# Optimization experiments

Hardware: AMD Instinct MI355X
Metric: run time of the kernel (lower is better)

The kernel has to match this reference:

```python
import jax, jax.numpy as jnp
import numpy as np

N_HEADS = 16
ROPE_BASE = 10000.0


def _apply_rope(t, cos, sin):
    # t: (B, H, S, D); cos/sin: (S, D/2). Rotate-half convention.
    d2 = t.shape[-1] // 2
    t1, t2 = t[..., :d2], t[..., d2:]
    return jnp.concatenate([t1 * cos - t2 * sin, t2 * cos + t1 * sin], axis=-1)


def setup_inputs() -> dict:
    key = jax.random.key(0)
    k0, k1, k2, k3, k4 = jax.random.split(key, 5)
    B, S, E = 4, 2048, 1024
    scale = 0.02
    x = jax.random.normal(k0, (B, S, E), dtype=jnp.float32)
    w_qkv = jax.random.normal(k1, (E, 3 * E), dtype=jnp.float32) * scale
    b_qkv = jnp.zeros((3 * E,), dtype=jnp.float32)
    w_proj = jax.random.normal(k2, (E, E), dtype=jnp.float32) * scale
    b_proj = jnp.zeros((E,), dtype=jnp.float32)
    return {"x": x, "w_qkv": w_qkv, "b_qkv": b_qkv, "w_proj": w_proj, "b_proj": b_proj}


def reference(x, w_qkv, b_qkv, w_proj, b_proj):
    B, S, E = x.shape
    H = N_HEADS
    D = E // H
    # fused QKV projection
    qkv = x @ w_qkv + b_qkv                      # (B, S, 3E)
    q, k, v = jnp.split(qkv, 3, axis=-1)
    def to_heads(t):
        return t.reshape(B, S, H, D).transpose(0, 2, 1, 3)  # (B, H, S, D)
    q, k, v = to_heads(q), to_heads(k), to_heads(v)
    # RoPE (rotate-half)
    inv_freq = ROPE_BASE ** (-jnp.arange(0, D, 2, dtype=jnp.float32) / D)  # (D/2,)
    pos = jnp.arange(S, dtype=jnp.float32)
    freqs = pos[:, None] * inv_freq[None, :]     # (S, D/2)
    cos, sin = jnp.cos(freqs), jnp.sin(freqs)
    q = _apply_rope(q, cos, sin)
    k = _apply_rope(k, cos, sin)
    # causal SDPA
    scores = jnp.einsum('bhqd,bhkd->bhqk', q, k) / jnp.sqrt(jnp.float32(D))
    causal = jnp.tril(jnp.ones((S, S), dtype=bool))
    scores = jnp.where(causal, scores, jnp.float32(-1e30))
    probs = jax.nn.softmax(scores, axis=-1)
    out = jnp.einsum('bhqk,bhkd->bhqd', probs, v)  # (B, H, S, D)
    out = out.transpose(0, 2, 1, 3).reshape(B, S, E)
    # output projection (dropout is identity at p=0 / eval)
    return out @ w_proj + b_proj
```

## Files before the change

### kernel.cpp

```cpp
#include <hip/hip_runtime.h>

typedef unsigned short u16;
typedef __bf16 bf16x8 __attribute__((ext_vector_type(8)));
typedef float f32x4 __attribute__((ext_vector_type(4)));

__device__ __forceinline__ u16 f2b(float f) {
    unsigned u = __builtin_bit_cast(unsigned, f);
    unsigned r = (u + 0x7fffu + ((u >> 16) & 1u)) >> 16;
    return (u16)r;
}
#if __has_builtin(__builtin_amdgcn_cvt_pk_bf16_f32)
typedef __bf16 bf16x2_t __attribute__((ext_vector_type(2)));
__device__ __forceinline__ unsigned pk2(float a, float b) {
    return __builtin_bit_cast(unsigned, __builtin_amdgcn_cvt_pk_bf16_f32(a, b));
}
#else
__device__ __forceinline__ unsigned pk2(float a, float b) {
    return (unsigned)f2b(a) | ((unsigned)f2b(b) << 16);
}
#endif
#if __has_builtin(__builtin_amdgcn_exp2f)
#define EXP2F(x) __builtin_amdgcn_exp2f(x)
#else
#define EXP2F(x) exp2f(x)
#endif

__device__ __forceinline__ void gl_lds16(const u16* g, u16* l) {
    __builtin_amdgcn_global_load_lds(
        (const __attribute__((address_space(1))) unsigned*)(const void*)g,
        (__attribute__((address_space(3))) unsigned*)(void*)l, 16, 0, 0);
}

__global__ __launch_bounds__(256) void k_rope_table(float2* __restrict__ tab) {
    int i = blockIdx.x * 256 + threadIdx.x;
    int s = i >> 5, d = i & 31;
    const float C0 = 0.4152410118609203f;
    float inv_freq = exp2f(-C0 * (float)d);
    float sn, cs;
    sincosf((float)s * inv_freq, &sn, &cs);
    tab[i] = make_float2(cs, sn);
}

__global__ __launch_bounds__(256) void k_convert(const float* __restrict__ in,
                                                 u16* __restrict__ out, int n8) {
    int i = blockIdx.x * 256 + threadIdx.x;
    if (i >= n8) return;
    const float4* p = (const float4*)(in + (size_t)i * 8);
    float4 a = p[0], b = p[1];
    u16 t[8] = {f2b(a.x), f2b(a.y), f2b(a.z), f2b(a.w),
                f2b(b.x), f2b(b.y), f2b(b.z), f2b(b.w)};
    *(uint4*)(out + (size_t)i * 8) = *(const uint4*)t;
}

__global__ __launch_bounds__(256) void k_transpose_bf16(const float* __restrict__ in,
                                                        u16* __restrict__ out,
                                                        int R, int C) {
    __shared__ u16 tile[64][72];
    int tc = blockIdx.x * 64;
    int tr = blockIdx.y * 64;
    for (int i = threadIdx.x; i < 4096; i += 256) {
        int r = i >> 6, c = i & 63;
        tile[c][r] = f2b(in[(size_t)(tr + r) * C + tc + c]);
    }
    __syncthreads();
    for (int i = threadIdx.x; i < 4096; i += 256) {
        int r = i >> 6, c = i & 63;
        out[(size_t)(tc + r) * R + tr + c] = tile[r][c];
    }
}

__device__ __forceinline__ void gemm_mainloop(const u16* __restrict__ Ab,
                                              const u16* __restrict__ Bb, int K,
                                              u16* As, u16* Bs, int tid,
                                              f32x4 (&acc)[4][4]) {
    const int wave = tid >> 6, lane = tid & 63;
    const int col = lane & 15, quad = lane >> 4;
    const int wm = wave >> 1, wn = wave & 1;
    const int lrow = lane >> 2, lk = (lane & 3) * 8;
    u16* ldsA0 = As + (wave * 16) * 32;
    u16* ldsA1 = As + (64 + wave * 16) * 32;
    u16* ldsB0 = Bs + (wave * 16) * 32;
    u16* ldsB1 = Bs + (64 + wave * 16) * 32;
    const u16* gA0 = Ab + (size_t)(wave * 16 + lrow) * K + lk;
    const u16* gA1 = gA0 + (size_t)64 * K;
    const u16* gB0 = Bb + (size_t)(wave * 16 + lrow) * K + lk;
    const u16* gB1 = gB0 + (size_t)64 * K;
    for (int k0 = 0; k0 < K; k0 += 64) {
        if (k0) __syncthreads();
#pragma unroll
        for (int kh = 0; kh < 2; ++kh) {
            int ko = k0 + kh * 32;
            gl_lds16(gA0 + ko, ldsA0 + kh * 4096);
            gl_lds16(gA1 + ko, ldsA1 + kh * 4096);
            gl_lds16(gB0 + ko, ldsB0 + kh * 4096);
            gl_lds16(gB1 + ko, ldsB1 + kh * 4096);
        }
        __syncthreads();
#pragma unroll
        for (int kh = 0; kh < 2; ++kh) {
            bf16x8 af[4], bfr[4];
#pragma unroll
            for (int mt = 0; mt < 4; ++mt)
                af[mt] = *(const bf16x8*)(As + kh * 4096 +
                                          (wm * 64 + mt * 16 + col) * 32 + quad * 8);
#pragma unroll
            for (int nt = 0; nt < 4; ++nt)
                bfr[nt] = *(const bf16x8*)(Bs + kh * 4096 +
                                           (wn * 64 + nt * 16 + col) * 32 + quad * 8);
#pragma unroll
            for (int mt = 0; mt < 4; ++mt)
#pragma unroll
                for (int nt = 0; nt < 4; ++nt)
                    acc[mt][nt] = __builtin_amdgcn_mfma_f32_16x16x32_bf16(
                        af[mt], bfr[nt], acc[mt][nt], 0, 0, 0);
        }
    }
}

__global__ __launch_bounds__(256) void k_gemm_qkv_rope(
    const u16* __restrict__ A, const u16* __restrict__ Bt,
    const float* __restrict__ bias, const float2* __restrict__ tab,
    u16* __restrict__ Qr, u16* __restrict__ Kr, u16* __restrict__ Vt) {
    __shared__ __align__(16) u16 smem[16384];
    u16* As = smem;
    u16* Bs = smem + 8192;
    const int K = 1024;
    int tid = threadIdx.x;
    int lane = tid & 63, wave = tid >> 6;
    int col = lane & 15, quad = lane >> 4;
    int wm = wave >> 1, wn = wave & 1;
    int mBase = blockIdx.y * 128;
    int nBase = blockIdx.x * 128;
    f32x4 acc[4][4] = {};
    gemm_mainloop(A + (size_t)mBase * K, Bt + (size_t)nBase * K, K, As, Bs, tid, acc);

    int region = nBase >> 10;
    int n64 = nBase + wn * 64;
    int h = (n64 & 1023) >> 6;
    if (region < 2) {
        __syncthreads();
        float qs = (region == 0) ? 0.18033688011112042f : 1.0f;
#pragma unroll
        for (int nt = 0; nt < 2; ++nt) {
            int d1 = nt * 16 + col;
            float b1 = bias[n64 + d1];
            float b2 = bias[n64 + d1 + 32];
            int nl = wn * 64 + nt * 16 + col;
#pragma unroll
            for (int mt = 0; mt < 4; ++mt) {
                int mlb = wm * 64 + mt * 16 + quad * 4;
#pragma unroll
                for (int r = 0; r < 4; ++r) {
                    int mloc = mlb + r;
                    int s = (mBase + mloc) & 2047;
                    float2 t = tab[s * 32 + d1];
                    float t1 = acc[mt][nt][r] + b1;
                    float t2 = acc[mt][nt + 2][r] + b2;
                    int sw = (mloc & 7) << 3;
                    smem[mloc * 128 + (nl ^ sw)] = f2b((t1 * t.x - t2 * t.y) * qs);
                    smem[mloc * 128 + ((nl + 32) ^ sw)] = f2b((t2 * t.x + t1 * t.y) * qs);
                }
            }
        }
        __syncthreads();
        u16* outp = (region == 0) ? Qr : Kr;
#pragma unroll
        for (int p = 0; p < 8; ++p) {
            int lin = p * 256 + tid;
            int mloc = lin >> 4;
            int c8 = (lin & 15) << 3;
            uint4 v = *(const uint4*)(smem + mloc * 128 + (c8 ^ ((mloc & 7) << 3)));
            int m = mBase + mloc;
            int s = m & 2047, b = m >> 11;
            int ng = (nBase & 1023) + c8;
            *(uint4*)(Qr == outp || Kr == outp
                          ? outp + ((size_t)((b * 16 + (ng >> 6)) * 2048 + s)) * 64 +
                                (ng & 63)
                          : outp) = v;
        }
    } else {
        int b = mBase >> 11;
        int sb0 = mBase & 2047;
#pragma unroll
        for (int nt = 0; nt < 4; ++nt) {
            int d = nt * 16 + col;
            float bv = bias[n64 + d];
            u16* vrow = Vt + ((size_t)((b * 16 + h) * 64 + d)) * 2048;
#pragma unroll
            for (int mt = 0; mt < 4; ++mt) {
                int s = sb0 + wm * 64 + mt * 16 + quad * 4;
                uint2 w;
                w.x = pk2(acc[mt][nt][0] + bv, acc[mt][nt][1] + bv);
                w.y = pk2(acc[mt][nt][2] + bv, acc[mt][nt][3] + bv);
                *(uint2*)(vrow + s) = w;
            }
        }
    }
}

__global__ __launch_bounds__(256) void k_attn(const u16* __restrict__ Qr,
                                              const u16* __restrict__ Kr,
                                              const u16* __restrict__ Vt,
                                              u16* __restrict__ O) {
    __shared__ __align__(16) u16 Ks[64 * 72];
    __shared__ __align__(16) u16 Vs[64 * 72];
    int tid = threadIdx.x, wave = tid >> 6, lane = tid & 63;
    int col = lane & 15, quad = lane >> 4;
    int bx = blockIdx.x, bh = blockIdx.y;
    int b = bh >> 4, h = bh & 15;
    size_t headQ = (size_t)bh * 2048 * 64;
    size_t headV = (size_t)bh * 64 * 2048;
    int r0 = tid >> 3, kc = tid & 7;
    int rb72 = ((col >> 2) * 8 + (col & 3)) * 72;

    for (int half = 0; half < 2; ++half) {
        int qb = half ? bx : (15 - bx);
        int t0 = 2 * qb, t1 = t0 + 1;
        int myq0 = qb * 128 + wave * 16 + col;
        int myq1 = myq0 + 64;
        const u16* qp0 = Qr + headQ + (size_t)myq0 * 64;
        const u16* qp1 = Qr + headQ + (size_t)myq1 * 64;
        bf16x8 aq00 = *(const bf16x8*)(qp0 + quad * 8);
        bf16x8 aq01 = *(const bf16x8*)(qp0 + 32 + quad * 8);
        bf16x8 aq10 = *(const bf16x8*)(qp1 + quad * 8);
        bf16x8 aq11 = *(const bf16x8*)(qp1 + 32 + quad * 8);
        f32x4 o0[4] = {}, o1[4] = {};
        float l0 = 0.f, l1 = 0.f;

        for (int j = 0; j <= t1; ++j) {
            bool d0 = (j <= t0);
            __syncthreads();
            {
                const u16* kg = Kr + headQ + (size_t)(j * 64 + r0) * 64 + kc * 8;
                const u16* vg = Vt + headV + (size_t)r0 * 2048 + j * 64 + kc * 8;
                *(uint4*)(Ks + r0 * 72 + kc * 8) = *(const uint4*)kg;
                *(uint4*)(Ks + (r0 + 32) * 72 + kc * 8) = *(const uint4*)(kg + 32 * 64);
                *(uint4*)(Vs + r0 * 72 + kc * 8) = *(const uint4*)vg;
                *(uint4*)(Vs + (r0 + 32) * 72 + kc * 8) = *(const uint4*)(vg + 32 * 2048);
            }
            __syncthreads();
            f32x4 s0[4], s1[4];
#pragma unroll
            for (int nt = 0; nt < 4; ++nt) {
                const u16* kp = Ks + rb72 + ((nt & 1) * 32 + (nt >> 1) * 4) * 72;
                bf16x8 ak0 = *(const bf16x8*)(kp + quad * 8);
                bf16x8 ak1 = *(const bf16x8*)(kp + 32 + quad * 8);
                if (d0) {
                    f32x4 z = {};
                    z = __builtin_amdgcn_mfma_f32_16x16x32_bf16(ak0, aq00, z, 0, 0, 0);
                    s0[nt] = __builtin_amdgcn_mfma_f32_16x16x32_bf16(ak1, aq01, z, 0, 0, 0);
                }
                f32x4 z = {};
                z = __builtin_amdgcn_mfma_f32_16x16x32_bf16(ak0, aq10, z, 0, 0, 0);
                s1[nt] = __builtin_amdgcn_mfma_f32_16x16x32_bf16(ak1, aq11, z, 0, 0, 0);
            }
            if (j == t0) {
#pragma unroll
                for (int nt = 0; nt < 4; ++nt) {
                    int keyb = j * 64 + (nt & 1) * 32 + quad * 8 + (nt >> 1) * 4;
#pragma unroll
                    for (int r = 0; r < 4; ++r)
                        if (keyb + r > myq0) s0[nt][r] = -3.0e38f;
                }
            }
            if (j == t1) {
#pragma unroll
                for (int nt = 0; nt < 4; ++nt) {
                    int keyb = j * 64 + (nt & 1) * 32 + quad * 8 + (nt >> 1) * 4;
#pragma unroll
                    for (int r = 0; r < 4; ++r)
                        if (keyb + r > myq1) s1[nt][r] = -3.0e38f;
                }
            }
            unsigned P40[8], P41[8];
            if (d0) {
#pragma unroll
                for (int nt = 0; nt < 4; ++nt) {
                    float p0 = EXP2F(s0[nt][0]);
                    float p1 = EXP2F(s0[nt][1]);
                    float p2 = EXP2F(s0[nt][2]);
                    float p3 = EXP2F(s0[nt][3]);
                    l0 += (p0 + p1) + (p2 + p3);
                    P40[2 * nt] = pk2(p0, p1);
                    P40[2 * nt + 1] = pk2(p2, p3);
                }
            }
#pragma unroll
            for (int nt = 0; nt < 4; ++nt) {
                float p0 = EXP2F(s1[nt][0]);
                float p1 = EXP2F(s1[nt][1]);
                float p2 = EXP2F(s1[nt][2]);
                float p3 = EXP2F(s1[nt][3]);
                l1 += (p0 + p1) + (p2 + p3);
                P41[2 * nt] = pk2(p0, p1);
                P41[2 * nt + 1] = pk2(p2, p3);
            }
#pragma unroll
            for (int kk = 0; kk < 2; ++kk) {
                uint4 bw0, bw1;
                bw0.x = P40[2 * kk];
                bw0.y = P40[2 * kk + 1];
                bw0.z = P40[2 * kk + 4];
                bw0.w = P40[2 * kk + 5];
                bw1.x = P41[2 * kk];
                bw1.y = P41[2 * kk + 1];
                bw1.z = P41[2 * kk + 4];
                bw1.w = P41[2 * kk + 5];
                bf16x8 bp0 = __builtin_bit_cast(bf16x8, bw0);
                bf16x8 bp1 = __builtin_bit_cast(bf16x8, bw1);
#pragma unroll
                for (int mt = 0; mt < 4; ++mt) {
                    bf16x8 av = *(const bf16x8*)(Vs + (mt * 16 + col) * 72 + kk * 32 + quad * 8);
                    if (d0)
                        o0[mt] = __builtin_amdgcn_mfma_f32_16x16x32_bf16(av, bp0, o0[mt], 0, 0, 0);
                    o1[mt] = __builtin_amdgcn_mfma_f32_16x16x32_bf16(av, bp1, o1[mt], 0, 0, 0);
                }
            }
        }
        l0 += __shfl_xor(l0, 16);
        l0 += __shfl_xor(l0, 32);
        l1 += __shfl_xor(l1, 16);
        l1 += __shfl_xor(l1, 32);
        float inv0 = 1.0f / l0, inv1 = 1.0f / l1;
        u16* orow0 = O + (size_t)(b * 2048 + myq0) * 1024 + h * 64;
        u16* orow1 = O + (size_t)(b * 2048 + myq1) * 1024 + h * 64;
#pragma unroll
        for (int mt = 0; mt < 4; ++mt) {
            uint2 w0, w1;
            w0.x = pk2(o0[mt][0] * inv0, o0[mt][1] * inv0);
            w0.y = pk2(o0[mt][2] * inv0, o0[mt][3] * inv0);
            w1.x = pk2(o1[mt][0] * inv1, o1[mt][1] * inv1);
            w1.y = pk2(o1[mt][2] * inv1, o1[mt][3] * inv1);
            *(uint2*)(orow0 + mt * 16 + quad * 4) = w0;
            *(uint2*)(orow1 + mt * 16 + quad * 4) = w1;
        }
    }
}

__global__ __launch_bounds__(256) void k_gemm_proj(const u16* __restrict__ A,
                                                   const u16* __restrict__ Bt,
                                                   const float* __restrict__ bias,
                                                   float* __restrict__ out) {
    __shared__ __align__(16) u16 As[2 * 128 * 32];
    __shared__ __align__(16) u16 Bs[2 * 128 * 32];
    const int K = 1024;
    int tid = threadIdx.x;
    int lane = tid & 63, wave = tid >> 6;
    int col = lane & 15, quad = lane >> 4;
    int wm = wave >> 1, wn = wave & 1;
    int mBase = blockIdx.y * 128;
    int nBase = blockIdx.x * 128;
    f32x4 acc[4][4] = {};
    gemm_mainloop(A + (size_t)mBase * K, Bt + (size_t)nBase * K, K, As, Bs, tid, acc);
#pragma unroll
    for (int nt = 0; nt < 4; ++nt) {
        int n = nBase + wn * 64 + nt * 16 + col;
        float bv = bias[n];
#pragma unroll
        for (int mt = 0; mt < 4; ++mt) {
            int m = mBase + wm * 64 + mt * 16 + quad * 4;
#pragma unroll
            for (int r = 0; r < 4; ++r)
                out[(size_t)(m + r) * 1024 + n] = acc[mt][nt][r] + bv;
        }
    }
}

extern "C" void kernel_launch(void* const* d_in, const int* in_sizes, int n_in,
                              void* d_out, int out_size, void* d_ws, size_t ws_size,
                              hipStream_t stream) {
    const float* x = (const float*)d_in[0];
    const float* w_qkv = (const float*)d_in[1];
    const float* b_qkv = (const float*)d_in[2];
    const float* w_proj = (const float*)d_in[3];
    const float* b_proj = (const float*)d_in[4];
    float* out = (float*)d_out;
    char* ws = (char*)d_ws;
    u16* x_bf = (u16*)(ws);
    u16* wqkvT = (u16*)(ws + 16777216);
    u16* wprojT = (u16*)(ws + 23068672);
    u16* Qr = (u16*)(ws + 25165824);
    u16* Kr = (u16*)(ws + 41943040);
    u16* Vt = (u16*)(ws + 58720256);
    u16* AO = (u16*)(ws + 75497472);
    float2* tab = (float2*)(ws + 75497472);

    k_rope_table<<<256, 256, 0, stream>>>(tab);
    k_convert<<<4096, 256, 0, stream>>>(x, x_bf, 1048576);
    k_transpose_bf16<<<dim3(48, 16), 256, 0, stream>>>(w_qkv, wqkvT, 1024, 3072);
    k_transpose_bf16<<<dim3(16, 16), 256, 0, stream>>>(w_proj, wprojT, 1024, 1024);
    k_gemm_qkv_rope<<<dim3(24, 64), 256, 0, stream>>>(x_bf, wqkvT, b_qkv, tab, Qr, Kr, Vt);
    k_attn<<<dim3(8, 64), 256, 0, stream>>>(Qr, Kr, Vt, AO);
    k_gemm_proj<<<dim3(8, 64), 256, 0, stream>>>(AO, wprojT, b_proj, out);
}
```

Before: 276.1 us.

## Double-buffer K/V tiles in attention and remap blocks per XCD and query tile

```diff
diff --git a/kernel.cpp b/kernel.cpp
--- a/kernel.cpp
+++ b/kernel.cpp
@@ -198,142 +198,166 @@
     }
 }
 
-__global__ __launch_bounds__(256) void k_attn(const u16* __restrict__ Qr,
-                                              const u16* __restrict__ Kr,
-                                              const u16* __restrict__ Vt,
-                                              u16* __restrict__ O) {
-    __shared__ __align__(16) u16 Ks[64 * 72];
-    __shared__ __align__(16) u16 Vs[64 * 72];
+__global__ __launch_bounds__(256, 4) void k_attn(const u16* __restrict__ Qr,
+                                                 const u16* __restrict__ Kr,
+                                                 const u16* __restrict__ Vt,
+                                                 u16* __restrict__ O) {
+    __shared__ __align__(16) u16 Ks[2][64 * 72];
+    __shared__ __align__(16) u16 Vs[2][64 * 72];
     int tid = threadIdx.x, wave = tid >> 6, lane = tid & 63;
     int col = lane & 15, quad = lane >> 4;
-    int bx = blockIdx.x, bh = blockIdx.y;
-    int b = bh >> 4, h = bh & 15;
-    size_t headQ = (size_t)bh * 2048 * 64;
-    size_t headV = (size_t)bh * 64 * 2048;
+    int id = blockIdx.x + (blockIdx.y << 4);
+    int xcd = id & 7, seq = id >> 3;
+    int head = xcd * 8 + (seq >> 4);
+    int qb = 15 - (seq & 15);
+    int b = head >> 4, h = head & 15;
+    size_t headQ = (size_t)head * 2048 * 64;
+    size_t headV = (size_t)head * 64 * 2048;
     int r0 = tid >> 3, kc = tid & 7;
     int rb72 = ((col >> 2) * 8 + (col & 3)) * 72;
 
-    for (int half = 0; half < 2; ++half) {
-        int qb = half ? bx : (15 - bx);
-        int t0 = 2 * qb, t1 = t0 + 1;
-        int myq0 = qb * 128 + wave * 16 + col;
-        int myq1 = myq0 + 64;
-        const u16* qp0 = Qr + headQ + (size_t)myq0 * 64;
-        const u16* qp1 = Qr + headQ + (size_t)myq1 * 64;
-        bf16x8 aq00 = *(const bf16x8*)(qp0 + quad * 8);
-        bf16x8 aq01 = *(const bf16x8*)(qp0 + 32 + quad * 8);
-        bf16x8 aq10 = *(const bf16x8*)(qp1 + quad * 8);
-        bf16x8 aq11 = *(const bf16x8*)(qp1 + 32 + quad * 8);
-        f32x4 o0[4] = {}, o1[4] = {};
-        float l0 = 0.f, l1 = 0.f;
-
-        for (int j = 0; j <= t1; ++j) {
-            bool d0 = (j <= t0);
+    int t0 = 2 * qb, t1 = t0 + 1;
+    int myq0 = qb * 128 + wave * 16 + col;
+    int myq1 = myq0 + 64;
+    const u16* qp0 = Qr + headQ + (size_t)myq0 * 64;
+    const u16* qp1 = Qr + headQ + (size_t)myq1 * 64;
+    bf16x8 aq00 = *(const bf16x8*)(qp0 + quad * 8);
+    bf16x8 aq01 = *(const bf16x8*)(qp0 + 32 + quad * 8);
+    bf16x8 aq10 = *(const bf16x8*)(qp1 + quad * 8);
+    bf16x8 aq11 = *(const bf16x8*)(qp1 + 32 + quad * 8);
+    f32x4 o0[4] = {}, o1[4] = {};
+    float l0 = 0.f, l1 = 0.f;
+
+    const u16* kg = Kr + headQ + (size_t)r0 * 64 + kc * 8;
+    const u16* vg = Vt + headV + (size_t)r0 * 2048 + kc * 8;
+    {
+        uint4 kr0 = *(const uint4*)kg;
+        uint4 kr1 = *(const uint4*)(kg + 32 * 64);
+        uint4 vr0 = *(const uint4*)vg;
+        uint4 vr1 = *(const uint4*)(vg + 32 * 2048);
+        *(uint4*)(Ks[0] + r0 * 72 + kc * 8) = kr0;
+        *(uint4*)(Ks[0] + (r0 + 32) * 72 + kc * 8) = kr1;
+        *(uint4*)(Vs[0] + r0 * 72 + kc * 8) = vr0;
+        *(uint4*)(Vs[0] + (r0 + 32) * 72 + kc * 8) = vr1;
+    }
+    __syncthreads();
+
+    for (int j = 0; j <= t1; ++j) {
+        int cur = j & 1;
+        uint4 kr0, kr1, vr0, vr1;
+        if (j < t1) {
+            const u16* kgn = kg + (size_t)(j + 1) * 64 * 64;
+            const u16* vgn = vg + (j + 1) * 64;
+            kr0 = *(const uint4*)kgn;
+            kr1 = *(const uint4*)(kgn + 32 * 64);
+            vr0 = *(const uint4*)vgn;
+            vr1 = *(const uint4*)(vgn + 32 * 2048);
+        }
+        bool d0 = (j <= t0);
+        const u16* KsC = Ks[cur];
+        const u16* VsC = Vs[cur];
+        f32x4 s0[4], s1[4];
+#pragma unroll
+        for (int nt = 0; nt < 4; ++nt) {
+            const u16* kp = KsC + rb72 + ((nt & 1) * 32 + (nt >> 1) * 4) * 72;
+            bf16x8 ak0 = *(const bf16x8*)(kp + quad * 8);
+            bf16x8 ak1 = *(const bf16x8*)(kp + 32 + quad * 8);
+            if (d0) {
+                f32x4 z = {};
+                z = __builtin_amdgcn_mfma_f32_16x16x32_bf16(ak0, aq00, z, 0, 0, 0);
+                s0[nt] = __builtin_amdgcn_mfma_f32_16x16x32_bf16(ak1, aq01, z, 0, 0, 0);
+            }
+            f32x4 z = {};
+            z = __builtin_amdgcn_mfma_f32_16x16x32_bf16(ak0, aq10, z, 0, 0, 0);
+            s1[nt] = __builtin_amdgcn_mfma_f32_16x16x32_bf16(ak1, aq11, z, 0, 0, 0);
+        }
+        if (j == t0) {
+#pragma unroll
+            for (int nt = 0; nt < 4; ++nt) {
+                int keyb = j * 64 + (nt & 1) * 32 + quad * 8 + (nt >> 1) * 4;
+#pragma unroll
+                for (int r = 0; r < 4; ++r)
+                    if (keyb + r > myq0) s0[nt][r] = -3.0e38f;
+            }
+        }
+        if (j == t1) {
+#pragma unroll
+            for (int nt = 0; nt < 4; ++nt) {
+                int keyb = j * 64 + (nt & 1) * 32 + quad * 8 + (nt >> 1) * 4;
+#pragma unroll
+                for (int r = 0; r < 4; ++r)
+                    if (keyb + r > myq1) s1[nt][r] = -3.0e38f;
+            }
+        }
+        unsigned P40[8], P41[8];
+        if (d0) {
+#pragma unroll
+            for (int nt = 0; nt < 4; ++nt) {
+                float p0 = EXP2F(s0[nt][0]);
+                float p1 = EXP2F(s0[nt][1]);
+                float p2 = EXP2F(s0[nt][2]);
+                float p3 = EXP2F(s0[nt][3]);
+                l0 += (p0 + p1) + (p2 + p3);
+                P40[2 * nt] = pk2(p0, p1);
+                P40[2 * nt + 1] = pk2(p2, p3);
+            }
+        }
+#pragma unroll
+        for (int nt = 0; nt < 4; ++nt) {
+            float p0 = EXP2F(s1[nt][0]);
+            float p1 = EXP2F(s1[nt][1]);
+            float p2 = EXP2F(s1[nt][2]);
+            float p3 = EXP2F(s1[nt][3]);
+            l1 += (p0 + p1) + (p2 + p3);
+            P41[2 * nt] = pk2(p0, p1);
+            P41[2 * nt + 1] = pk2(p2, p3);
+        }
+#pragma unroll
+        for (int kk = 0; kk < 2; ++kk) {
+            uint4 bw0, bw1;
+            bw0.x = P40[2 * kk];
+            bw0.y = P40[2 * kk + 1];
+            bw0.z = P40[2 * kk + 4];
+            bw0.w = P40[2 * kk + 5];
+            bw1.x = P41[2 * kk];
+            bw1.y = P41[2 * kk + 1];
+            bw1.z = P41[2 * kk + 4];
+            bw1.w = P41[2 * kk + 5];
+            bf16x8 bp0 = __builtin_bit_cast(bf16x8, bw0);
+            bf16x8 bp1 = __builtin_bit_cast(bf16x8, bw1);
+#pragma unroll
+            for (int mt = 0; mt < 4; ++mt) {
+                bf16x8 av = *(const bf16x8*)(VsC + (mt * 16 + col) * 72 + kk * 32 + quad * 8);
+                if (d0)
+                    o0[mt] = __builtin_amdgcn_mfma_f32_16x16x32_bf16(av, bp0, o0[mt], 0, 0, 0);
+                o1[mt] = __builtin_amdgcn_mfma_f32_16x16x32_bf16(av, bp1, o1[mt], 0, 0, 0);
+            }
+        }
+        if (j < t1) {
+            int nxt = cur ^ 1;
+            *(uint4*)(Ks[nxt] + r0 * 72 + kc * 8) = kr0;
+            *(uint4*)(Ks[nxt] + (r0 + 32) * 72 + kc * 8) = kr1;
+            *(uint4*)(Vs[nxt] + r0 * 72 + kc * 8) = vr0;
+            *(uint4*)(Vs[nxt] + (r0 + 32) * 72 + kc * 8) = vr1;
             __syncthreads();
-            {
-                const u16* kg = Kr + headQ + (size_t)(j * 64 + r0) * 64 + kc * 8;
-                const u16* vg = Vt + headV + (size_t)r0 * 2048 + j * 64 + kc * 8;
-                *(uint4*)(Ks + r0 * 72 + kc * 8) = *(const uint4*)kg;
-                *(uint4*)(Ks + (r0 + 32) * 72 + kc * 8) = *(const uint4*)(kg + 32 * 64);
-                *(uint4*)(Vs + r0 * 72 + kc * 8) = *(const uint4*)vg;
-                *(uint4*)(Vs + (r0 + 32) * 72 + kc * 8) = *(const uint4*)(vg + 32 * 2048);
-            }
-            __syncthreads();
-            f32x4 s0[4], s1[4];
-#pragma unroll
-            for (int nt = 0; nt < 4; ++nt) {
-                const u16* kp = Ks + rb72 + ((nt & 1) * 32 + (nt >> 1) * 4) * 72;
-                bf16x8 ak0 = *(const bf16x8*)(kp + quad * 8);
-                bf16x8 ak1 = *(const bf16x8*)(kp + 32 + quad * 8);
-                if (d0) {
-                    f32x4 z = {};
-                    z = __builtin_amdgcn_mfma_f32_16x16x32_bf16(ak0, aq00, z, 0, 0, 0);
-                    s0[nt] = __builtin_amdgcn_mfma_f32_16x16x32_bf16(ak1, aq01, z, 0, 0, 0);
-                }
-                f32x4 z = {};
-                z = __builtin_amdgcn_mfma_f32_16x16x32_bf16(ak0, aq10, z, 0, 0, 0);
-                s1[nt] = __builtin_amdgcn_mfma_f32_16x16x32_bf16(ak1, aq11, z, 0, 0, 0);
-            }
-            if (j == t0) {
-#pragma unroll
-                for (int nt = 0; nt < 4; ++nt) {
-                    int keyb = j * 64 + (nt & 1) * 32 + quad * 8 + (nt >> 1) * 4;
-#pragma unroll
-                    for (int r = 0; r < 4; ++r)
-                        if (keyb + r > myq0) s0[nt][r] = -3.0e38f;
-                }
-            }
-            if (j == t1) {
-#pragma unroll
-                for (int nt = 0; nt < 4; ++nt) {
-                    int keyb = j * 64 + (nt & 1) * 32 + quad * 8 + (nt >> 1) * 4;
-#pragma unroll
-                    for (int r = 0; r < 4; ++r)
-                        if (keyb + r > myq1) s1[nt][r] = -3.0e38f;
-                }
-            }
-            unsigned P40[8], P41[8];
-            if (d0) {
-#pragma unroll
-                for (int nt = 0; nt < 4; ++nt) {
-                    float p0 = EXP2F(s0[nt][0]);
-                    float p1 = EXP2F(s0[nt][1]);
-                    float p2 = EXP2F(s0[nt][2]);
-                    float p3 = EXP2F(s0[nt][3]);
-                    l0 += (p0 + p1) + (p2 + p3);
-                    P40[2 * nt] = pk2(p0, p1);
-                    P40[2 * nt + 1] = pk2(p2, p3);
-                }
-            }
-#pragma unroll
-            for (int nt = 0; nt < 4; ++nt) {
-                float p0 = EXP2F(s1[nt][0]);
-                float p1 = EXP2F(s1[nt][1]);
-                float p2 = EXP2F(s1[nt][2]);
-                float p3 = EXP2F(s1[nt][3]);
-                l1 += (p0 + p1) + (p2 + p3);
-                P41[2 * nt] = pk2(p0, p1);
-                P41[2 * nt + 1] = pk2(p2, p3);
-            }
-#pragma unroll
-            for (int kk = 0; kk < 2; ++kk) {
-                uint4 bw0, bw1;
-                bw0.x = P40[2 * kk];
-                bw0.y = P40[2 * kk + 1];
-                bw0.z = P40[2 * kk + 4];
-                bw0.w = P40[2 * kk + 5];
-                bw1.x = P41[2 * kk];
-                bw1.y = P41[2 * kk + 1];
-                bw1.z = P41[2 * kk + 4];
-                bw1.w = P41[2 * kk + 5];
-                bf16x8 bp0 = __builtin_bit_cast(bf16x8, bw0);
-                bf16x8 bp1 = __builtin_bit_cast(bf16x8, bw1);
-#pragma unroll
-                for (int mt = 0; mt < 4; ++mt) {
-                    bf16x8 av = *(const bf16x8*)(Vs + (mt * 16 + col) * 72 + kk * 32 + quad * 8);
-                    if (d0)
-                        o0[mt] = __builtin_amdgcn_mfma_f32_16x16x32_bf16(av, bp0, o0[mt], 0, 0, 0);
-                    o1[mt] = __builtin_amdgcn_mfma_f32_16x16x32_bf16(av, bp1, o1[mt], 0, 0, 0);
-                }
-            }
-        }
-        l0 += __shfl_xor(l0, 16);
-        l0 += __shfl_xor(l0, 32);
-        l1 += __shfl_xor(l1, 16);
-        l1 += __shfl_xor(l1, 32);
-        float inv0 = 1.0f / l0, inv1 = 1.0f / l1;
-        u16* orow0 = O + (size_t)(b * 2048 + myq0) * 1024 + h * 64;
-        u16* orow1 = O + (size_t)(b * 2048 + myq1) * 1024 + h * 64;
-#pragma unroll
-        for (int mt = 0; mt < 4; ++mt) {
-            uint2 w0, w1;
-            w0.x = pk2(o0[mt][0] * inv0, o0[mt][1] * inv0);
-            w0.y = pk2(o0[mt][2] * inv0, o0[mt][3] * inv0);
-            w1.x = pk2(o1[mt][0] * inv1, o1[mt][1] * inv1);
-            w1.y = pk2(o1[mt][2] * inv1, o1[mt][3] * inv1);
-            *(uint2*)(orow0 + mt * 16 + quad * 4) = w0;
-            *(uint2*)(orow1 + mt * 16 + quad * 4) = w1;
-        }
+        }
+    }
+    l0 += __shfl_xor(l0, 16);
+    l0 += __shfl_xor(l0, 32);
+    l1 += __shfl_xor(l1, 16);
+    l1 += __shfl_xor(l1, 32);
+    float inv0 = 1.0f / l0, inv1 = 1.0f / l1;
+    u16* orow0 = O + (size_t)(b * 2048 + myq0) * 1024 + h * 64;
+    u16* orow1 = O + (size_t)(b * 2048 + myq1) * 1024 + h * 64;
+#pragma unroll
+    for (int mt = 0; mt < 4; ++mt) {
+        uint2 w0, w1;
+        w0.x = pk2(o0[mt][0] * inv0, o0[mt][1] * inv0);
+        w0.y = pk2(o0[mt][2] * inv0, o0[mt][3] * inv0);
+        w1.x = pk2(o1[mt][0] * inv1, o1[mt][1] * inv1);
+        w1.y = pk2(o1[mt][2] * inv1, o1[mt][3] * inv1);
+        *(uint2*)(orow0 + mt * 16 + quad * 4) = w0;
+        *(uint2*)(orow1 + mt * 16 + quad * 4) = w1;
     }
 }
 
@@ -390,6 +414,6 @@
     k_transpose_bf16<<<dim3(48, 16), 256, 0, stream>>>(w_qkv, wqkvT, 1024, 3072);
     k_transpose_bf16<<<dim3(16, 16), 256, 0, stream>>>(w_proj, wprojT, 1024, 1024);
     k_gemm_qkv_rope<<<dim3(24, 64), 256, 0, stream>>>(x_bf, wqkvT, b_qkv, tab, Qr, Kr, Vt);
-    k_attn<<<dim3(8, 64), 256, 0, stream>>>(Qr, Kr, Vt, AO);
+    k_attn<<<dim3(16, 64), 256, 0, stream>>>(Qr, Kr, Vt, AO);
     k_gemm_proj<<<dim3(8, 64), 256, 0, stream>>>(AO, wprojT, b_proj, out);
 }
```

Result: no change. 280.4 us (+1.6%).
